# Optimization experiments

Hardware: AMD Instinct MI355X
Metric: run time of the kernel (lower is better)

## Reference

```python
import jax, jax.numpy as jnp
import numpy as np
from jax import lax

D_MODEL = 96
EXPAND = 2.66
D_INNER = int(EXPAND * D_MODEL)  # 255
DT_RANK = -(-D_MODEL // 16)      # 6
D_STATE = 8
K = 4                            # 4 scan directions
WIN = 8
NCLUST = 16
B, H, W = 2, 64, 64
N = H * W
L = 2 * N                        # opt/sar interleaved


def setup_inputs() -> dict:
    key = jax.random.key(0)
    ks = jax.random.split(key, 16)
    s = 0.05
    def rn(i, shape):
        return jax.random.normal(ks[i], shape, jnp.float32) * s
    # dt bias init: inv-softplus of dt ~ LogUniform[1e-3, 1e-1]
    dt = jnp.exp(jax.random.uniform(ks[10], (K, D_INNER)) * (np.log(0.1) - np.log(0.001)) + np.log(0.001))
    dt = jnp.clip(dt, 1e-4, None)
    inv_dt = dt + jnp.log(-jnp.expm1(-dt))
    A_logs = jnp.log(jnp.tile(jnp.arange(1, D_STATE + 1, dtype=jnp.float32)[None, :], (K * D_INNER, 1)))
    return dict(
        optical=jax.random.normal(ks[0], (B, D_MODEL, H, W), jnp.float32),
        sar=jax.random.normal(ks[1], (B, D_MODEL, H, W), jnp.float32),
        anchor_idx=jax.random.randint(ks[2], (B, NCLUST), 0, N),
        in_w_opt=rn(3, (2 * D_INNER, D_MODEL)),
        in_w_sar=rn(4, (2 * D_INNER, D_MODEL)),
        conv_w_opt=rn(5, (D_INNER, 1, 3, 3)),
        conv_b_opt=rn(6, (D_INNER,)),
        conv_w_sar=rn(7, (D_INNER, 1, 3, 3)),
        conv_b_sar=rn(8, (D_INNER,)),
        x_proj_weight=rn(9, (K, DT_RANK + 2 * D_STATE, D_INNER)),
        dt_projs_weight=rn(11, (K, D_INNER, DT_RANK)),
        dt_projs_bias=inv_dt.astype(jnp.float32),
        A_logs=A_logs,
        Ds=jnp.ones((K * D_INNER,), jnp.float32),
        ln_w_opt=jnp.ones((D_INNER,), jnp.float32),
        ln_b_opt=jnp.zeros((D_INNER,), jnp.float32),
        ln_w_sar=jnp.ones((D_INNER,), jnp.float32),
        ln_b_sar=jnp.zeros((D_INNER,), jnp.float32),
        out_w_opt=rn(12, (D_MODEL, D_INNER)),
        out_w_sar=rn(13, (D_MODEL, D_INNER)),
    )


def _dwconv(x, w, b):
    # depthwise 3x3, SAME padding; x: (B, D_INNER, H, W), w: (D_INNER, 1, 3, 3)
    y = lax.conv_general_dilated(x, w, (1, 1), [(1, 1), (1, 1)],
                                 dimension_numbers=('NCHW', 'OIHW', 'NCHW'),
                                 feature_group_count=D_INNER)
    return y + b[None, :, None, None]


def _ln(x, w, b):
    m = jnp.mean(x, -1, keepdims=True)
    v = jnp.mean((x - m) ** 2, -1, keepdims=True)
    return (x - m) * lax.rsqrt(v + 1e-5) * w + b


def _patches(x, order):
    # x: (B, C, H, W) -> (B, C, N) in one of 4 window-scan orders
    b, c, h, w_ = x.shape
    p = x.reshape(b, c, h // WIN, WIN, w_ // WIN, WIN)
    if order in ('ltr_utd', 'rtl_dtu'):
        p = p.transpose(0, 1, 2, 4, 3, 5)
    else:
        p = p.transpose(0, 1, 4, 2, 5, 3)
    if order in ('rtl_dtu', 'dtu_rtl'):
        p = jnp.flip(p, (2, 3, 4, 5))
    return p.reshape(b, c, -1)


def _selective_scan(u, delta, A, Bm, Cm, Ds2, bias):
    # u, delta: (B,K,C,L); A: (K,C,Ns); Bm, Cm: (B,K,Ns,L); Ds2, bias: (K,C)
    delta = jax.nn.softplus(delta + bias[None, :, :, None])
    u_l = jnp.moveaxis(u, 3, 0)      # (L,B,K,C)
    d_l = jnp.moveaxis(delta, 3, 0)
    B_l = jnp.moveaxis(Bm, 3, 0)     # (L,B,K,Ns)
    C_l = jnp.moveaxis(Cm, 3, 0)
    h0 = jnp.zeros(u.shape[:3] + (A.shape[-1],), u.dtype)  # (B,K,C,Ns)
    def step(h, inp):
        ut, dt, bt, ct = inp
        h = h * jnp.exp(dt[..., None] * A) + (dt * ut)[..., None] * bt[:, :, None, :]
        y = jnp.einsum('bkcn,bkn->bkc', h, ct)
        return h, y
    _, ys = lax.scan(step, h0, (u_l, d_l, B_l, C_l))
    return jnp.moveaxis(ys, 0, 3) + u * Ds2[None, :, :, None]


def _forward(optical, sar, in_w_opt, in_w_sar, conv_w_opt, conv_b_opt, conv_w_sar,
             conv_b_sar, x_proj_weight, dt_projs_weight, dt_projs_bias, A_logs, Ds,
             ln_w_opt, ln_b_opt, ln_w_sar, ln_b_sar, out_w_opt, out_w_sar, anchor_idx):
    C = D_INNER
    x_opt = optical.transpose(0, 2, 3, 1)  # (B,H,W,D_MODEL)
    x_sar = sar.transpose(0, 2, 3, 1)
    xo, zo = jnp.split(x_opt @ in_w_opt.T, 2, axis=-1)
    xs_, zs = jnp.split(x_sar @ in_w_sar.T, 2, axis=-1)
    xo = jax.nn.silu(_dwconv(xo.transpose(0, 3, 1, 2), conv_w_opt, conv_b_opt))   # (B,C,H,W)
    xs_ = jax.nn.silu(_dwconv(xs_.transpose(0, 3, 1, 2), conv_w_sar, conv_b_sar))
    # --- cluster-sorted token reorder ---
    xof = xo.reshape(B, C, N).transpose(0, 2, 1)   # (B,N,C)
    xsf = xs_.reshape(B, C, N).transpose(0, 2, 1)
    anchors = jnp.take_along_axis(xof, jnp.broadcast_to(anchor_idx[:, :, None], (B, NCLUST, C)), axis=1)
    d2 = (jnp.sum(xof ** 2, -1)[:, :, None] + jnp.sum(anchors ** 2, -1)[:, None, :]
          - 2.0 * jnp.einsum('bnc,bmc->bnm', xof, anchors))
    assign = jnp.argmin(d2, axis=2)            # (B,N)
    sorted_idx = jnp.argsort(assign, axis=1)
    inv_idx = jnp.argsort(sorted_idx, axis=1)
    go = jnp.take_along_axis(xof, jnp.broadcast_to(sorted_idx[:, :, None], xof.shape), 1).transpose(0, 2, 1).reshape(B, C, H, W)
    gs = jnp.take_along_axis(xsf, jnp.broadcast_to(sorted_idx[:, :, None], xsf.shape), 1).transpose(0, 2, 1).reshape(B, C, H, W)
    # --- 4-direction window scans, opt/sar interleaved ---
    seqs = []
    for order in ('ltr_utd', 'rtl_dtu', 'utd_ltr', 'dtu_rtl'):
        po = _patches(go, order)
        ps = _patches(gs, order)
        seqs.append(jnp.stack([po, ps], axis=-1).reshape(B, C, L))
    xs4 = jnp.stack(seqs, axis=1)  # (B,K,C,L)
    x_dbl = jnp.einsum('bkdl,kcd->bkcl', xs4, x_proj_weight)
    dts, Bs, Cs = jnp.split(x_dbl, [DT_RANK, DT_RANK + D_STATE], axis=2)
    dts = jnp.einsum('bkrl,kdr->bkdl', dts, dt_projs_weight)
    A = -jnp.exp(A_logs).reshape(K, D_INNER, D_STATE)
    out_y = _selective_scan(xs4, dts, A, Bs, Cs, Ds.reshape(K, D_INNER), dt_projs_bias)  # (B,K,C,L)
    y = jnp.sum(out_y, axis=1)                 # (B,C,L)
    yo = y[:, :, 0::2] / K                     # (B,C,N)
    ysr = y[:, :, 1::2] / K
    yo = jnp.take_along_axis(yo, jnp.broadcast_to(inv_idx[:, None, :], yo.shape), 2)
    ysr = jnp.take_along_axis(ysr, jnp.broadcast_to(inv_idx[:, None, :], ysr.shape), 2)
    yo = yo.transpose(0, 2, 1).reshape(B, H, W, C)
    ysr = ysr.transpose(0, 2, 1).reshape(B, H, W, C)
    yo = _ln(yo, ln_w_opt, ln_b_opt) * jax.nn.silu(zo)
    ysr = _ln(ysr, ln_w_sar, ln_b_sar) * jax.nn.silu(zs)
    out_opt = (yo @ out_w_opt.T).transpose(0, 3, 1, 2)
    out_sar = (ysr @ out_w_sar.T).transpose(0, 3, 1, 2)
    return out_opt, out_sar


def reference(optical, sar, in_w_opt, in_w_sar, conv_w_opt, conv_b_opt, conv_w_sar,
              conv_b_sar, x_proj_weight, dt_projs_weight, dt_projs_bias, A_logs, Ds,
              ln_w_opt, ln_b_opt, ln_w_sar, ln_b_sar, out_w_opt, out_w_sar, anchor_idx):
    return _forward(optical, sar, in_w_opt, in_w_sar, conv_w_opt, conv_b_opt, conv_w_sar,
                    conv_b_sar, x_proj_weight, dt_projs_weight, dt_projs_bias, A_logs, Ds,
                    ln_w_opt, ln_b_opt, ln_w_sar, ln_b_sar, out_w_opt, out_w_sar, anchor_idx)
```

## Files before the change

### kernel.cpp

```cpp
#include <hip/hip_runtime.h>
#include <math.h>

#define DM 96
#define DI 255
#define GSTR 256
#define NS 8
#define RK 6
#define NK 4
#define NB 2
#define NT 4096
#define LL 8192
#define NCL 16
#define GRP 16
#define NCH 512
#define NG (NCH / GRP)
#define CLN (NT / NCH)

__device__ __forceinline__ float sigm(float x) { return 1.f / (1.f + __expf(-x)); }

__global__ __launch_bounds__(256) void k_inproj(
    const float* __restrict__ opt, const float* __restrict__ sar,
    const float* __restrict__ w_o, const float* __restrict__ w_s,
    float* __restrict__ xpre_o, float* __restrict__ xpre_s,
    float* __restrict__ sz_o, float* __restrict__ sz_s)
{
  int tile = blockIdx.x;
  int oc = blockIdx.y & 1, m = blockIdx.y >> 1;
  int b = blockIdx.z;
  const float* inp = m ? sar : opt;
  const float* W   = m ? w_s : w_o;
  float* xp        = m ? xpre_s : xpre_o;
  float* szp       = m ? sz_s : sz_o;
  int n0 = tile * 64, c0 = oc * 256;
  __shared__ float xin[96 * 68];
  __shared__ float Wl[48 * 260];
  int tid = threadIdx.x;
  for (int idx = tid; idx < 96 * 64; idx += 256) {
    int d = idx >> 6, tk = idx & 63;
    xin[d * 68 + tk] = inp[(size_t)(b * DM + d) * NT + n0 + tk];
  }
  int tokg = tid & 7, og = tid >> 3;
  int tok0 = tokg * 8, o0 = og * 8;
  float acc[8][8];
#pragma unroll
  for (int j = 0; j < 8; ++j)
#pragma unroll
    for (int t = 0; t < 8; ++t) acc[j][t] = 0.f;
  for (int ks = 0; ks < 2; ++ks) {
    __syncthreads();
    {
      int row = c0 + tid; if (row > 509) row = 509;
      const float4* wg = (const float4*)(W + (size_t)row * 96 + ks * 48);
#pragma unroll
      for (int q = 0; q < 12; ++q) {
        float4 v = wg[q];
        Wl[(q * 4 + 0) * 260 + tid] = v.x;
        Wl[(q * 4 + 1) * 260 + tid] = v.y;
        Wl[(q * 4 + 2) * 260 + tid] = v.z;
        Wl[(q * 4 + 3) * 260 + tid] = v.w;
      }
    }
    __syncthreads();
    for (int dd = 0; dd < 48; ++dd) {
      int d = ks * 48 + dd;
      float4 xa = *(const float4*)&xin[d * 68 + tok0];
      float4 xb = *(const float4*)&xin[d * 68 + tok0 + 4];
      float4 wa = *(const float4*)&Wl[dd * 260 + o0];
      float4 wb = *(const float4*)&Wl[dd * 260 + o0 + 4];
      float xs8[8] = {xa.x, xa.y, xa.z, xa.w, xb.x, xb.y, xb.z, xb.w};
      float ws8[8] = {wa.x, wa.y, wa.z, wa.w, wb.x, wb.y, wb.z, wb.w};
#pragma unroll
      for (int j = 0; j < 8; ++j)
#pragma unroll
        for (int t = 0; t < 8; ++t) acc[j][t] = fmaf(ws8[j], xs8[t], acc[j][t]);
    }
  }
#pragma unroll
  for (int j = 0; j < 8; ++j) {
    int oo = c0 + o0 + j;
    if (oo < DI) {
      float4 v0 = make_float4(acc[j][0], acc[j][1], acc[j][2], acc[j][3]);
      float4 v1 = make_float4(acc[j][4], acc[j][5], acc[j][6], acc[j][7]);
      float* dst = xp + ((size_t)b * DI + oo) * NT + n0 + tok0;
      *(float4*)dst = v0;
      *(float4*)(dst + 4) = v1;
    } else if (oo < 510) {
      int cz = oo - DI;
#pragma unroll
      for (int t = 0; t < 8; ++t) {
        float v = acc[j][t];
        szp[((size_t)b * NT + n0 + tok0 + t) * GSTR + cz] = v * sigm(v);
      }
    }
  }
}

__global__ __launch_bounds__(256) void k_conv(
    const float* __restrict__ xpre_o, const float* __restrict__ xpre_s,
    const float* __restrict__ cw_o, const float* __restrict__ cb_o,
    const float* __restrict__ cw_s, const float* __restrict__ cb_s,
    float* __restrict__ G_o, float* __restrict__ G_s)
{
  int h = blockIdx.x & 63, cg = blockIdx.x >> 6;
  int m = blockIdx.y, b = blockIdx.z;
  const float* xp = m ? xpre_s : xpre_o;
  const float* cw = m ? cw_s : cw_o;
  const float* cb = m ? cb_s : cb_o;
  float* G = m ? G_s : G_o;
  int c0 = cg * 64;
  __shared__ float wts[64 * 9];
  __shared__ float bia[64];
  __shared__ float ot[64 * 65];
  int tid = threadIdx.x;
  for (int i = tid; i < 64 * 9; i += 256) {
    int c = c0 + i / 9;
    wts[i] = (c < DI) ? cw[c * 9 + i % 9] : 0.f;
  }
  if (tid < 64) bia[tid] = (c0 + tid < DI) ? cb[c0 + tid] : 0.f;
  __syncthreads();
  int w = tid & 63, g = tid >> 6;
  for (int t = 0; t < 16; ++t) {
    int ci = g * 16 + t;
    int c = c0 + ci;
    float a = bia[ci];
    if (c < DI) {
      const float* pl = xp + ((size_t)b * DI + c) * NT;
#pragma unroll
      for (int dh = -1; dh <= 1; ++dh) {
        int hh = h + dh;
        if (hh < 0 || hh >= 64) continue;
#pragma unroll
        for (int dw = -1; dw <= 1; ++dw) {
          int w2 = w + dw;
          if (w2 < 0 || w2 >= 64) continue;
          a = fmaf(pl[hh * 64 + w2], wts[ci * 9 + (dh + 1) * 3 + (dw + 1)], a);
        }
      }
    }
    ot[ci * 65 + w] = a * sigm(a);
  }
  __syncthreads();
  int c = c0 + w;
  if (c < DI) {
    for (int jj = 0; jj < 16; ++jj) {
      int j = g * 16 + jj;
      G[((size_t)b * NT + h * 64 + j) * GSTR + c] = ot[w * 65 + j];
    }
  } else if (c == DI) {
    for (int jj = 0; jj < 16; ++jj) {
      int j = g * 16 + jj;
      G[((size_t)b * NT + h * 64 + j) * GSTR + c] = 0.f;
    }
  }
}

__global__ __launch_bounds__(256) void k_cluster(
    const float* __restrict__ G_o, const int* __restrict__ aidx,
    int* __restrict__ assign)
{
  int tile = blockIdx.x, b = blockIdx.y;
  __shared__ float anch[NCL * 260];
  __shared__ float anrm[NCL];
  int tid = threadIdx.x;
  for (int idx = tid; idx < NCL * 256; idx += 256) {
    int mm = idx >> 8, c = idx & 255;
    anch[mm * 260 + c] = (c < DI)
        ? G_o[((size_t)b * NT + aidx[b * NCL + mm]) * GSTR + c] : 0.f;
  }
  __syncthreads();
  if (tid < NCL) {
    float s = 0.f;
    for (int c = 0; c < DI; ++c) { float v = anch[tid * 260 + c]; s = fmaf(v, v, s); }
    anrm[tid] = s;
  }
  __syncthreads();
  int lane = tid & 63, wv = tid >> 6;
  int mm = lane & 15, tg = lane >> 4;
  for (int p = 0; p < 2; ++p) {
    int n = tile * 32 + p * 16 + wv * 4 + tg;
    const float* row = G_o + ((size_t)b * NT + n) * GSTR;
    float dot = 0.f;
#pragma unroll 8
    for (int cb = 0; cb < 64; ++cb) {
      float4 x4 = *(const float4*)(row + cb * 4);
      float4 a4 = *(const float4*)&anch[mm * 260 + cb * 4];
      dot = fmaf(x4.x, a4.x, dot);
      dot = fmaf(x4.y, a4.y, dot);
      dot = fmaf(x4.z, a4.z, dot);
      dot = fmaf(x4.w, a4.w, dot);
    }
    float score = anrm[mm] - 2.f * dot;
    int bi = mm;
#pragma unroll
    for (int off = 1; off < 16; off <<= 1) {
      float os = __shfl_xor(score, off, 64);
      int oi = __shfl_xor(bi, off, 64);
      if (os < score || (os == score && oi < bi)) { score = os; bi = oi; }
    }
    if (mm == 0) assign[b * NT + n] = bi;
  }
}

__global__ __launch_bounds__(256) void k_sort(
    const int* __restrict__ assign, int* __restrict__ sorted)
{
  int b = blockIdx.x;
  __shared__ int cnt[NCL];
  __shared__ int base[NCL];
  __shared__ int wcnt[4][NCL];
  int tid = threadIdx.x;
  if (tid < NCL) cnt[tid] = 0;
  __syncthreads();
  for (int ch = 0; ch < 16; ++ch) atomicAdd(&cnt[assign[b * NT + ch * 256 + tid]], 1);
  __syncthreads();
  if (tid == 0) {
    int run = 0;
    for (int mm = 0; mm < NCL; ++mm) { base[mm] = run; run += cnt[mm]; }
  }
  __syncthreads();
  int lane = tid & 63, wv = tid >> 6;
  for (int ch = 0; ch < 16; ++ch) {
    int n = ch * 256 + tid;
    int a = assign[b * NT + n];
    unsigned long long mymask = 0;
    for (int mm = 0; mm < NCL; ++mm) {
      unsigned long long msk = __ballot(a == mm);
      if (a == mm) mymask = msk;
      if (lane == mm) wcnt[wv][mm] = __popcll(msk);
    }
    __syncthreads();
    int before = 0;
    for (int w2 = 0; w2 < 4; ++w2) if (w2 < wv) before += wcnt[w2][a];
    before += __popcll(mymask & ((1ull << lane) - 1ull));
    sorted[b * NT + base[a] + before] = n;
    __syncthreads();
    if (tid < NCL) base[tid] += wcnt[0][tid] + wcnt[1][tid] + wcnt[2][tid] + wcnt[3][tid];
    __syncthreads();
  }
}

__global__ __launch_bounds__(256) void k_stok(
    const int* __restrict__ sorted, int* __restrict__ stok)
{
  int idx = blockIdx.x * 256 + threadIdx.x;
  int n = idx & (NT - 1);
  int k = (idx >> 12) & 3;
  int b = idx >> 14;
  int nn = (k & 1) ? (NT - 1 - n) : n;
  int tok;
  if (k < 2) {
    int hb = (nn >> 9) & 7, wb = (nn >> 6) & 7, hi = (nn >> 3) & 7, wi = nn & 7;
    tok = ((hb << 3) + hi) * 64 + (wb << 3) + wi;
  } else {
    int wb = (nn >> 9) & 7, hb = (nn >> 6) & 7, wi = (nn >> 3) & 7, hi = nn & 7;
    tok = ((hb << 3) + hi) * 64 + (wb << 3) + wi;
  }
  stok[idx] = sorted[b * NT + tok];
}

__global__ __launch_bounds__(256) void k_xdbl(
    const float* __restrict__ G_o, const float* __restrict__ G_s,
    const int* __restrict__ stok, const float* __restrict__ xpw,
    float* __restrict__ xdbl)
{
  int lt = blockIdx.x, k = blockIdx.y, b = blockIdx.z;
  int l0 = lt * 32;
  __shared__ float xt[32 * 260];
  __shared__ float Wl[22 * 260];
  int tid = threadIdx.x;
  int lane = tid & 63, wv = tid >> 6;
  for (int i = tid; i < 22 * 256; i += 256) {
    int r = i >> 8, c = i & 255;
    Wl[r * 260 + c] = (c < DI) ? xpw[(k * 22 + r) * DI + c] : 0.f;
  }
  for (int rr = 0; rr < 8; ++rr) {
    int i = wv * 8 + rr;
    int l = l0 + i;
    int n = l >> 1;
    int j = stok[((b * NK + k) << 12) + n];
    const float* row = ((l & 1) ? G_s : G_o) + ((size_t)b * NT + j) * GSTR;
    float4 v = *(const float4*)(row + lane * 4);
    *(float4*)&xt[i * 260 + lane * 4] = v;
  }
  __syncthreads();
  int ll = tid & 31, rq = tid >> 5;
  const float* xr = &xt[ll * 260];
  const float* w0 = &Wl[rq * 260];
  const float* w1 = &Wl[(rq + 8) * 260];
  bool has2 = (rq < 6);
  const float* w2 = &Wl[(has2 ? rq + 16 : rq) * 260];
  float a0 = 0.f, a1 = 0.f, a2 = 0.f;
#pragma unroll 8
  for (int c4 = 0; c4 < 64; ++c4) {
    float4 x4 = *(const float4*)(xr + c4 * 4);
    float4 u0 = *(const float4*)(w0 + c4 * 4);
    float4 u1 = *(const float4*)(w1 + c4 * 4);
    float4 u2 = *(const float4*)(w2 + c4 * 4);
    a0 = fmaf(x4.x, u0.x, a0); a0 = fmaf(x4.y, u0.y, a0);
    a0 = fmaf(x4.z, u0.z, a0); a0 = fmaf(x4.w, u0.w, a0);
    a1 = fmaf(x4.x, u1.x, a1); a1 = fmaf(x4.y, u1.y, a1);
    a1 = fmaf(x4.z, u1.z, a1); a1 = fmaf(x4.w, u1.w, a1);
    a2 = fmaf(x4.x, u2.x, a2); a2 = fmaf(x4.y, u2.y, a2);
    a2 = fmaf(x4.z, u2.z, a2); a2 = fmaf(x4.w, u2.w, a2);
  }
  float* o = xdbl + (((size_t)(b * NK + k) * LL) + l0 + ll) * 22;
  o[rq] = a0;
  o[rq + 8] = a1;
  if (has2) o[rq + 16] = a2;
}

template <int PHASE>
__global__ __launch_bounds__(256) void k_scan(
    const float* __restrict__ G_o, const float* __restrict__ G_s,
    const int* __restrict__ stok, const int* __restrict__ sorted,
    const float* __restrict__ xdbl,
    const float* __restrict__ dtw, const float* __restrict__ dtb,
    const float* __restrict__ Dsp, const float* __restrict__ hst,
    float* __restrict__ summ, float* __restrict__ Y_o, float* __restrict__ Y_s)
{
  int ch = blockIdx.x, b = blockIdx.y;
  int tid = threadIdx.x;
  int c = tid < DI ? tid : DI - 1;
  bool act = tid < DI;
  float wdt[NK][RK], bias[NK], dd[NK], st[NK][NS], S[NK];
#pragma unroll
  for (int k = 0; k < NK; ++k) {
    int rc = k * DI + c;
#pragma unroll
    for (int r = 0; r < RK; ++r) wdt[k][r] = dtw[rc * RK + r];
    bias[k] = dtb[rc];
    S[k] = 0.f;
    if (PHASE == 3) {
      dd[k] = Dsp[rc];
#pragma unroll
      for (int nn = 0; nn < NS; ++nn)
        st[k][nn] = hst[((((size_t)b * NCH + ch) * NK + k) * NS + nn) * DI + c];
    } else {
      dd[k] = 0.f;
#pragma unroll
      for (int nn = 0; nn < NS; ++nn) st[k][nn] = 0.f;
    }
  }
  for (int ni = 0; ni < CLN; ++ni) {
    int n = ch * CLN + ni;
    int jk[NK];
#pragma unroll
    for (int k = 0; k < NK; ++k) jk[k] = stok[((b * NK + k) << 12) + n];
    int jo = 0;
    if (PHASE == 3) jo = sorted[b * NT + n];
#pragma unroll
    for (int m = 0; m < 2; ++m) {
      const float* G = m ? G_s : G_o;
      int l = 2 * n + m;
      float ys = 0.f;
#pragma unroll
      for (int k = 0; k < NK; ++k) {
        float u = G[((size_t)b * NT + jk[k]) * GSTR + c];
        const float* xd = xdbl + ((size_t)(b * NK + k) * LL + l) * 22;
        float draw = bias[k];
#pragma unroll
        for (int r = 0; r < RK; ++r) draw = fmaf(xd[r], wdt[k][r], draw);
        float dlt = fmaxf(draw, 0.f) + __logf(1.f + __expf(-fabsf(draw)));
        if (PHASE == 1) S[k] += dlt;
        float e1 = __expf(-dlt);
        float e2 = e1 * e1, e3 = e2 * e1, e4 = e2 * e2;
        float e5 = e4 * e1, e6 = e4 * e2, e7 = e6 * e1, e8 = e4 * e4;
        float p8[NS] = {e1, e2, e3, e4, e5, e6, e7, e8};
        float du = dlt * u;
        float yk = 0.f;
#pragma unroll
        for (int nn = 0; nn < NS; ++nn) {
          st[k][nn] = fmaf(st[k][nn], p8[nn], du * xd[6 + nn]);
          if (PHASE == 3) yk = fmaf(st[k][nn], xd[14 + nn], yk);
        }
        if (PHASE == 3) ys += yk + u * dd[k];
      }
      if (PHASE == 3 && act) {
        float* Y = m ? Y_s : Y_o;
        Y[((size_t)b * NT + jo) * GSTR + c] = 0.25f * ys;
      }
    }
  }
  if (PHASE == 1 && act) {
#pragma unroll
    for (int k = 0; k < NK; ++k) {
      size_t bb = (((size_t)b * NCH + ch) * NK + k) * 9;
#pragma unroll
      for (int nn = 0; nn < NS; ++nn) summ[(bb + nn) * DI + c] = st[k][nn];
      summ[(bb + 8) * DI + c] = S[k];
    }
  }
}

__global__ __launch_bounds__(256) void k_comb_a(
    const float* __restrict__ summ, float* __restrict__ Aagg,
    float* __restrict__ Qagg)
{
  int g = blockIdx.x, yb = blockIdx.y;
  int nn = yb & 7, k = (yb >> 3) & 3, b = yb >> 5;
  int tid = threadIdx.x;
  int c = tid < DI ? tid : DI - 1;
  float fn = (float)(nn + 1);
  int ch0 = g * GRP;
  float q[GRP], S[GRP];
#pragma unroll
  for (int j = 0; j < GRP; ++j) {
    size_t bb = (((size_t)b * NCH + ch0 + j) * NK + k) * 9;
    q[j] = summ[(bb + nn) * DI + c];
    S[j] = summ[(bb + 8) * DI + c];
  }
  float A = 1.f, Q = 0.f;
#pragma unroll
  for (int j = 0; j < GRP; ++j) {
    float a = __expf(-S[j] * fn);
    Q = fmaf(a, Q, q[j]);
    A *= a;
  }
  if (tid < DI) {
    Aagg[((size_t)yb * NG + g) * DI + c] = A;
    Qagg[((size_t)yb * NG + g) * DI + c] = Q;
  }
}

__global__ __launch_bounds__(256) void k_comb_b(
    const float* __restrict__ Aagg, const float* __restrict__ Qagg,
    float* __restrict__ Hgrp)
{
  int yb = blockIdx.x;
  int tid = threadIdx.x;
  int c = tid < DI ? tid : DI - 1;
  bool act = tid < DI;
  float Av[NG], Qv[NG];
#pragma unroll
  for (int g = 0; g < NG; ++g) {
    Av[g] = Aagg[((size_t)yb * NG + g) * DI + c];
    Qv[g] = Qagg[((size_t)yb * NG + g) * DI + c];
  }
  float H = 0.f;
#pragma unroll
  for (int g = 0; g < NG; ++g) {
    if (act) Hgrp[((size_t)yb * NG + g) * DI + c] = H;
    H = fmaf(Av[g], H, Qv[g]);
  }
}

__global__ __launch_bounds__(256) void k_comb_c(
    const float* __restrict__ summ, const float* __restrict__ Hgrp,
    float* __restrict__ hst)
{
  int g = blockIdx.x, yb = blockIdx.y;
  int nn = yb & 7, k = (yb >> 3) & 3, b = yb >> 5;
  int tid = threadIdx.x;
  int c = tid < DI ? tid : DI - 1;
  bool act = tid < DI;
  float fn = (float)(nn + 1);
  int ch0 = g * GRP;
  float q[GRP], S[GRP];
#pragma unroll
  for (int j = 0; j < GRP; ++j) {
    size_t bb = (((size_t)b * NCH + ch0 + j) * NK + k) * 9;
    q[j] = summ[(bb + nn) * DI + c];
    S[j] = summ[(bb + 8) * DI + c];
  }
  float h = Hgrp[((size_t)yb * NG + g) * DI + c];
#pragma unroll
  for (int j = 0; j < GRP; ++j) {
    if (act)
      hst[((((size_t)b * NCH + ch0 + j) * NK + k) * NS + nn) * DI + c] = h;
    float a = __expf(-S[j] * fn);
    h = fmaf(a, h, q[j]);
  }
}

__global__ __launch_bounds__(256) void k_final(
    const float* __restrict__ Y_o, const float* __restrict__ Y_s,
    const float* __restrict__ sz_o, const float* __restrict__ sz_s,
    const float* __restrict__ lnw_o, const float* __restrict__ lnb_o,
    const float* __restrict__ lnw_s, const float* __restrict__ lnb_s,
    const float* __restrict__ ow_o, const float* __restrict__ ow_s,
    float* __restrict__ out)
{
  int tile = blockIdx.x, m = blockIdx.y, b = blockIdx.z;
  const float* Y   = m ? Y_s : Y_o;
  const float* szp = m ? sz_s : sz_o;
  const float* lnw = m ? lnw_s : lnw_o;
  const float* lnb = m ? lnb_s : lnb_o;
  const float* Wo  = m ? ow_s : ow_o;
  float* outp = out + ((size_t)m * NB + b) * DM * NT;
  int n0 = tile * 64;
  __shared__ float gt[64 * 68];
  __shared__ float Wl[64 * 100];
  __shared__ float mean_s[64], rstd_s[64];
  __shared__ float lnwv[256], lnbv[256];
  int tid = threadIdx.x;
  if (tid < 256) {
    lnwv[tid] = (tid < DI) ? lnw[tid] : 0.f;
    lnbv[tid] = (tid < DI) ? lnb[tid] : 0.f;
  }
  int lane = tid & 63, wv = tid >> 6;
  for (int t = 0; t < 16; ++t) {
    int tk = wv * 16 + t;
    const float* yr = Y + ((size_t)b * NT + n0 + tk) * GSTR;
    float v0 = yr[lane], v1 = yr[lane + 64], v2 = yr[lane + 128];
    float v3 = (lane < 63) ? yr[lane + 192] : 0.f;
    float s1 = v0 + v1 + v2 + v3;
    float s2 = v0 * v0 + v1 * v1 + v2 * v2 + v3 * v3;
#pragma unroll
    for (int o = 1; o < 64; o <<= 1) {
      s1 += __shfl_xor(s1, o, 64);
      s2 += __shfl_xor(s2, o, 64);
    }
    if (lane == 0) {
      float mean = s1 * (1.f / DI);
      float var = s2 * (1.f / DI) - mean * mean;
      mean_s[tk] = mean;
      rstd_s[tk] = rsqrtf(var + 1e-5f);
    }
  }
  __syncthreads();
  int tokg = tid & 15, dg = tid >> 4;
  int t0 = tokg * 4, d0 = dg * 6;
  float acc[6][4];
#pragma unroll
  for (int j = 0; j < 6; ++j)
#pragma unroll
    for (int t = 0; t < 4; ++t) acc[j][t] = 0.f;
  for (int cc0 = 0; cc0 < 256; cc0 += 64) {
    {
      int tok = tid & 63, cgq = tid >> 6;
      const float* yr = Y + ((size_t)b * NT + n0 + tok) * GSTR;
      const float* zr = szp + ((size_t)b * NT + n0 + tok) * GSTR;
      float mn = mean_s[tok], rs = rstd_s[tok];
      for (int i = 0; i < 16; ++i) {
        int c = cc0 + cgq * 16 + i;
        float g = 0.f;
        if (c < DI) g = ((yr[c] - mn) * rs * lnwv[c] + lnbv[c]) * zr[c];
        gt[(cgq * 16 + i) * 68 + tok] = g;
      }
    }
    for (int i = tid; i < 96 * 64; i += 256) {
      int d = i >> 6, cl = i & 63;
      int c = cc0 + cl;
      Wl[cl * 100 + d] = (c < DI) ? Wo[d * DI + c] : 0.f;
    }
    __syncthreads();
    for (int cl = 0; cl < 64; ++cl) {
      float4 g4 = *(const float4*)&gt[cl * 68 + t0];
      const float2* wp = (const float2*)&Wl[cl * 100 + d0];
      float2 wa = wp[0], wb = wp[1], wc2 = wp[2];
      float wv6[6] = {wa.x, wa.y, wb.x, wb.y, wc2.x, wc2.y};
      float gv[4] = {g4.x, g4.y, g4.z, g4.w};
#pragma unroll
      for (int j = 0; j < 6; ++j)
#pragma unroll
        for (int t = 0; t < 4; ++t) acc[j][t] = fmaf(wv6[j], gv[t], acc[j][t]);
    }
    __syncthreads();
  }
#pragma unroll
  for (int j = 0; j < 6; ++j) {
    float4 v = make_float4(acc[j][0], acc[j][1], acc[j][2], acc[j][3]);
    *(float4*)(outp + (size_t)(d0 + j) * NT + n0 + t0) = v;
  }
}

extern "C" void kernel_launch(void* const* d_in, const int* in_sizes, int n_in,
                              void* d_out, int out_size, void* d_ws, size_t ws_size,
                              hipStream_t stream)
{
  (void)in_sizes; (void)n_in; (void)out_size; (void)ws_size;
  const float* opt    = (const float*)d_in[0];
  const float* sar    = (const float*)d_in[1];
  const int*   aidx   = (const int*)d_in[2];
  const float* w_in_o = (const float*)d_in[3];
  const float* w_in_s = (const float*)d_in[4];
  const float* cw_o   = (const float*)d_in[5];
  const float* cb_o   = (const float*)d_in[6];
  const float* cw_s   = (const float*)d_in[7];
  const float* cb_s   = (const float*)d_in[8];
  const float* xpw    = (const float*)d_in[9];
  const float* dtw    = (const float*)d_in[10];
  const float* dtb    = (const float*)d_in[11];
  const float* Dsp    = (const float*)d_in[13];
  const float* lnw_o  = (const float*)d_in[14];
  const float* lnb_o  = (const float*)d_in[15];
  const float* lnw_s  = (const float*)d_in[16];
  const float* lnb_s  = (const float*)d_in[17];
  const float* ow_o   = (const float*)d_in[18];
  const float* ow_s   = (const float*)d_in[19];
  float* out = (float*)d_out;

  char* wsb = (char*)d_ws;
  size_t off = 0;
  auto take = [&](size_t nbytes) {
    char* p = wsb + off;
    off += (nbytes + 255) & ~(size_t)255;
    return p;
  };
  float* xpre_o = (float*)take(sizeof(float) * (size_t)NB * NT * GSTR);
  float* xpre_s = (float*)take(sizeof(float) * (size_t)NB * NT * GSTR);
  float* G_o    = (float*)take(sizeof(float) * (size_t)NB * NT * GSTR);
  float* G_s    = (float*)take(sizeof(float) * (size_t)NB * NT * GSTR);
  float* sz_o   = (float*)take(sizeof(float) * (size_t)NB * NT * GSTR);
  float* sz_s   = (float*)take(sizeof(float) * (size_t)NB * NT * GSTR);
  float* xdbl   = (float*)take(sizeof(float) * (size_t)NB * NK * LL * 22);
  int* assign   = (int*)take(sizeof(int) * NB * NT);
  int* sorted   = (int*)take(sizeof(int) * NB * NT);
  int* stok     = (int*)take(sizeof(int) * NB * NK * NT);
  float* summ = (float*)take(sizeof(float) * (size_t)NB * NCH * NK * 9 * DI);
  float* hst  = (float*)take(sizeof(float) * (size_t)NB * NCH * NK * NS * DI);
  float* Aagg = (float*)take(sizeof(float) * (size_t)64 * NG * DI);
  float* Qagg = (float*)take(sizeof(float) * (size_t)64 * NG * DI);
  float* Hgrp = (float*)take(sizeof(float) * (size_t)64 * NG * DI);
  float* Y_o = xpre_o;
  float* Y_s = xpre_s;

  k_inproj<<<dim3(64, 4, NB), 256, 0, stream>>>(opt, sar, w_in_o, w_in_s,
                                                xpre_o, xpre_s, sz_o, sz_s);
  k_conv<<<dim3(256, 2, NB), 256, 0, stream>>>(xpre_o, xpre_s, cw_o, cb_o, cw_s, cb_s, G_o, G_s);
  k_cluster<<<dim3(128, NB), 256, 0, stream>>>(G_o, aidx, assign);
  k_sort<<<NB, 256, 0, stream>>>(assign, sorted);
  k_stok<<<NB * NK * 16, 256, 0, stream>>>(sorted, stok);
  k_xdbl<<<dim3(256, NK, NB), 256, 0, stream>>>(G_o, G_s, stok, xpw, xdbl);
  k_scan<1><<<dim3(NCH, NB), 256, 0, stream>>>(G_o, G_s, stok, sorted, xdbl, dtw, dtb,
                                               Dsp, nullptr, summ, nullptr, nullptr);
  k_comb_a<<<dim3(NG, 64), 256, 0, stream>>>(summ, Aagg, Qagg);
  k_comb_b<<<64, 256, 0, stream>>>(Aagg, Qagg, Hgrp);
  k_comb_c<<<dim3(NG, 64), 256, 0, stream>>>(summ, Hgrp, hst);
  k_scan<3><<<dim3(NCH, NB), 256, 0, stream>>>(G_o, G_s, stok, sorted, xdbl, dtw, dtb,
                                               Dsp, hst, nullptr, Y_o, Y_s);
  k_final<<<dim3(64, 2, NB), 256, 0, stream>>>(Y_o, Y_s, sz_o, sz_s,
                                               lnw_o, lnb_o, lnw_s, lnb_s, ow_o, ow_s, out);
}
```

Before: 297.9 us.

## Restructure final LN+out-proj kernel: smaller token tiles, single-pass gated LN

The final kernel now handles 32 tokens per block instead of 64, which doubles the grid to 512 blocks. Each wave reads Y and z once with coalesced loads, computes LayerNorm stats in registers, and writes the full gated activation tile for all 256 channels to shared memory up front. The old version read Y twice, once for the stats and again per channel chunk, with strided per-thread loads. The trade-off is that the out-projection weights are now reloaded for every 32 tokens rather than every 64, and each thread does a smaller 3x4 register tile.

Result: faster. 280.2 us (-6.0%).

```diff
diff --git a/kernel.cpp b/kernel.cpp
--- a/kernel.cpp
+++ b/kernel.cpp
@@ -487,78 +487,77 @@
   const float* lnb = m ? lnb_s : lnb_o;
   const float* Wo  = m ? ow_s : ow_o;
   float* outp = out + ((size_t)m * NB + b) * DM * NT;
-  int n0 = tile * 64;
-  __shared__ float gt[64 * 68];
-  __shared__ float Wl[64 * 100];
-  __shared__ float mean_s[64], rstd_s[64];
-  __shared__ float lnwv[256], lnbv[256];
-  int tid = threadIdx.x;
-  if (tid < 256) {
-    lnwv[tid] = (tid < DI) ? lnw[tid] : 0.f;
-    lnbv[tid] = (tid < DI) ? lnb[tid] : 0.f;
-  }
+  int n0 = tile * 32;
+  __shared__ float gt[256 * 36];
+  __shared__ float Wl[64 * 98];
+  int tid = threadIdx.x;
   int lane = tid & 63, wv = tid >> 6;
-  for (int t = 0; t < 16; ++t) {
-    int tk = wv * 16 + t;
-    const float* yr = Y + ((size_t)b * NT + n0 + tk) * GSTR;
-    float v0 = yr[lane], v1 = yr[lane + 64], v2 = yr[lane + 128];
-    float v3 = (lane < 63) ? yr[lane + 192] : 0.f;
-    float s1 = v0 + v1 + v2 + v3;
-    float s2 = v0 * v0 + v1 * v1 + v2 * v2 + v3 * v3;
+  float lnwv[4], lnbv[4];
+#pragma unroll
+  for (int q = 0; q < 4; ++q) {
+    int c = lane + 64 * q;
+    lnwv[q] = (c < DI) ? lnw[c] : 0.f;
+    lnbv[q] = (c < DI) ? lnb[c] : 0.f;
+  }
+  for (int t = 0; t < 8; ++t) {
+    int tok = wv * 8 + t;
+    const float* yr = Y + ((size_t)b * NT + n0 + tok) * GSTR;
+    const float* zr = szp + ((size_t)b * NT + n0 + tok) * GSTR;
+    float yv[4], zv[4];
+#pragma unroll
+    for (int q = 0; q < 4; ++q) {
+      int c = lane + 64 * q;
+      bool ok = (c < DI);
+      yv[q] = ok ? yr[c] : 0.f;
+      zv[q] = ok ? zr[c] : 0.f;
+    }
+    float s1 = yv[0] + yv[1] + yv[2] + yv[3];
+    float s2 = yv[0] * yv[0] + yv[1] * yv[1] + yv[2] * yv[2] + yv[3] * yv[3];
 #pragma unroll
     for (int o = 1; o < 64; o <<= 1) {
       s1 += __shfl_xor(s1, o, 64);
       s2 += __shfl_xor(s2, o, 64);
     }
-    if (lane == 0) {
-      float mean = s1 * (1.f / DI);
-      float var = s2 * (1.f / DI) - mean * mean;
-      mean_s[tk] = mean;
-      rstd_s[tk] = rsqrtf(var + 1e-5f);
-    }
-  }
-  __syncthreads();
-  int tokg = tid & 15, dg = tid >> 4;
-  int t0 = tokg * 4, d0 = dg * 6;
-  float acc[6][4];
-#pragma unroll
-  for (int j = 0; j < 6; ++j)
+    float mean = s1 * (1.f / DI);
+    float var = s2 * (1.f / DI) - mean * mean;
+    float rstd = rsqrtf(var + 1e-5f);
+#pragma unroll
+    for (int q = 0; q < 4; ++q) {
+      int c = lane + 64 * q;
+      float g = (c < DI) ? ((yv[q] - mean) * rstd * lnwv[q] + lnbv[q]) * zv[q] : 0.f;
+      gt[c * 36 + tok] = g;
+    }
+  }
+  int tokg = tid & 7, dg = tid >> 3;
+  int t0 = tokg * 4, d0 = dg * 3;
+  float acc[3][4];
+#pragma unroll
+  for (int j = 0; j < 3; ++j)
 #pragma unroll
     for (int t = 0; t < 4; ++t) acc[j][t] = 0.f;
   for (int cc0 = 0; cc0 < 256; cc0 += 64) {
-    {
-      int tok = tid & 63, cgq = tid >> 6;
-      const float* yr = Y + ((size_t)b * NT + n0 + tok) * GSTR;
-      const float* zr = szp + ((size_t)b * NT + n0 + tok) * GSTR;
-      float mn = mean_s[tok], rs = rstd_s[tok];
-      for (int i = 0; i < 16; ++i) {
-        int c = cc0 + cgq * 16 + i;
-        float g = 0.f;
-        if (c < DI) g = ((yr[c] - mn) * rs * lnwv[c] + lnbv[c]) * zr[c];
-        gt[(cgq * 16 + i) * 68 + tok] = g;
-      }
-    }
+    __syncthreads();
     for (int i = tid; i < 96 * 64; i += 256) {
       int d = i >> 6, cl = i & 63;
       int c = cc0 + cl;
-      Wl[cl * 100 + d] = (c < DI) ? Wo[d * DI + c] : 0.f;
+      Wl[cl * 98 + d] = (c < DI) ? Wo[d * DI + c] : 0.f;
     }
     __syncthreads();
     for (int cl = 0; cl < 64; ++cl) {
-      float4 g4 = *(const float4*)&gt[cl * 68 + t0];
-      const float2* wp = (const float2*)&Wl[cl * 100 + d0];
-      float2 wa = wp[0], wb = wp[1], wc2 = wp[2];
-      float wv6[6] = {wa.x, wa.y, wb.x, wb.y, wc2.x, wc2.y};
+      float4 g4 = *(const float4*)&gt[(cc0 + cl) * 36 + t0];
+      const float* wr = &Wl[cl * 98 + d0];
+      float w0 = wr[0], w1 = wr[1], w2 = wr[2];
       float gv[4] = {g4.x, g4.y, g4.z, g4.w};
 #pragma unroll
-      for (int j = 0; j < 6; ++j)
-#pragma unroll
-        for (int t = 0; t < 4; ++t) acc[j][t] = fmaf(wv6[j], gv[t], acc[j][t]);
-    }
-    __syncthreads();
-  }
-#pragma unroll
-  for (int j = 0; j < 6; ++j) {
+      for (int t = 0; t < 4; ++t) {
+        acc[0][t] = fmaf(w0, gv[t], acc[0][t]);
+        acc[1][t] = fmaf(w1, gv[t], acc[1][t]);
+        acc[2][t] = fmaf(w2, gv[t], acc[2][t]);
+      }
+    }
+  }
+#pragma unroll
+  for (int j = 0; j < 3; ++j) {
     float4 v = make_float4(acc[j][0], acc[j][1], acc[j][2], acc[j][3]);
     *(float4*)(outp + (size_t)(d0 + j) * NT + n0 + t0) = v;
   }
@@ -629,6 +628,6 @@
   k_comb_c<<<dim3(NG, 64), 256, 0, stream>>>(summ, Hgrp, hst);
   k_scan<3><<<dim3(NCH, NB), 256, 0, stream>>>(G_o, G_s, stok, sorted, xdbl, dtw, dtb,
                                                Dsp, hst, nullptr, Y_o, Y_s);
-  k_final<<<dim3(64, 2, NB), 256, 0, stream>>>(Y_o, Y_s, sz_o, sz_s,
-                                               lnw_o, lnb_o, lnw_s, lnb_s, ow_o, ow_s, out);
-}
+  k_final<<<dim3(128, 2, NB), 256, 0, stream>>>(Y_o, Y_s, sz_o, sz_s,
+                                                lnw_o, lnb_o, lnw_s, lnb_s, ow_o, ow_s, out);
+}
```
